# Optimization experiments

Measured on AMD Instinct MI355X. Metric: run time of the kernel, lower is better.

## Reference

```python
import jax, jax.numpy as jnp
import numpy as np

N_QUBITS = 12
N_LAYERS = 3


def _apply_ry(state, theta, q):
    # state: (2,)*n real statevector; RY on qubit q
    c = jnp.cos(theta * 0.5)
    s = jnp.sin(theta * 0.5)
    st = jnp.moveaxis(state, q, 0)
    st = jnp.stack([c * st[0] - s * st[1], s * st[0] + c * st[1]])
    return jnp.moveaxis(st, 0, q)


def _apply_cz(state, q, r):
    st = jnp.moveaxis(state, (q, r), (0, 1))
    st = st.at[1, 1].multiply(-1.0)
    return jnp.moveaxis(st, (0, 1), (q, r))


def _embed(x, params):
    # angle-embedding ansatz: L layers of RY(theta[l,q]+x[q]) + CZ ring
    n = N_QUBITS
    state = jnp.zeros((2,) * n, dtype=x.dtype).at[(0,) * n].set(1.0)
    for l in range(N_LAYERS):
        for q in range(n):
            state = _apply_ry(state, params[l, q] + x[q], q)
        for q in range(n):
            state = _apply_cz(state, q, (q + 1) % n)
    return state.reshape(-1)  # (2^n,)


def setup_inputs() -> dict:
    key = jax.random.key(0)
    k1, k2, k3 = jax.random.split(key, 3)
    data = jax.random.uniform(k1, (2048, N_QUBITS), dtype=jnp.float32)
    labels = jax.random.randint(k2, (2048,), 0, 2, dtype=jnp.int32)
    params = jax.random.normal(k3, (N_LAYERS, N_QUBITS), dtype=jnp.float32)
    return {"data": data, "labels": labels, "params": params}


def reference(data, labels, params):
    # Psi[i] = U(x_i, params)|0>, k_ij = |<psi_j|psi_i>|^2 (== prob of amp 0 of U^dag(x_j)U(x_i)|0>)
    psi = jax.vmap(_embed, in_axes=(0, None))(data, params)  # (N, 2^n)
    K = jnp.square(psi @ psi.T)                              # (N, N) pairwise kernel
    lab = 2.0 * labels.astype(psi.dtype) - 1.0               # {0,1} -> {-1,+1}
    LL = jnp.outer(lab, lab)
    kernel_polarity = jnp.sum(LL * K)
    square_sum_k = jnp.sum(K * K)
    square_sum_l = jnp.sum(LL * LL)
    return kernel_polarity / jnp.sqrt(square_sum_k * square_sum_l)
```

## Files before the change

### kernel.cpp

```cpp
#include <hip/hip_runtime.h>
#include <math.h>

#define NQ    12
#define DIM   4096
#define K_EXT 4096
#define KSL   512
#define NSAMP 2048
#define NLAY  3
#define NT2   16
#define NTRI2 136
#define NSLICE 8
#define BK    64

typedef __attribute__((ext_vector_type(8)))  short bf16x8;
typedef __attribute__((ext_vector_type(16))) float floatx16;

__device__ __forceinline__ unsigned short f32_to_bf16(float x) {
    unsigned u = __builtin_bit_cast(unsigned, x);
    u += 0x7FFFu + ((u >> 16) & 1u);
    return (unsigned short)(u >> 16);
}

__device__ __forceinline__ void gl_lds16(const unsigned short* g, unsigned short* l) {
    __builtin_amdgcn_global_load_lds(
        (const __attribute__((address_space(1))) unsigned int*)g,
        (__attribute__((address_space(3))) unsigned int*)l,
        16, 0, 0);
}

__device__ __forceinline__ void tri_decode(int bid, int& bi, int& bj) {
    int i = (int)((33.0 - sqrt(33.0*33.0 - 8.0*(double)bid)) * 0.5);
    int start = i*(33-i)/2;
    while (bid < start)               { --i; start = i*(33-i)/2; }
    while (bid >= start + (NT2 - i))  { start += NT2 - i; ++i; }
    bi = i; bj = i + (bid - start);
}

__global__ __launch_bounds__(256) void sim_kernel(const float* __restrict__ data,
                                                  const float* __restrict__ params,
                                                  unsigned short* __restrict__ pe)
{
    __shared__ float CS[2*36], SN[2*36];
    __shared__ float trans[2][4608];
    const int tid  = threadIdx.x;
    const int wave = tid >> 6, lane = tid & 63;
    const int sidx = wave >> 1;
    const int w    = wave & 1;
    const int smp  = blockIdx.x * 2 + sidx;

    if (w == 0 && lane < NLAY*NQ) {
        const int q = lane % NQ;
        const float th = 0.5f * (params[lane] + data[smp*NQ + q]);
        CS[sidx*36 + lane] = cosf(th);
        SN[sidx*36 + lane] = sinf(th);
    }
    __syncthreads();

    float v[32];
    #pragma unroll
    for (int r = 0; r < 32; ++r) v[r] = 0.f;
    if (w == 0 && lane == 0) v[0] = 1.f;

    float* buf = trans[sidx];
    float* wb  = buf + 36*lane + 2304*w;
    const float* rb = buf + ((lane>>2)&15) + 16*w + 36*(lane&3);

    #pragma unroll 1
    for (int l = 0; l < NLAY; ++l) {
        const float* cs = &CS[sidx*36 + l*NQ];
        const float* sn = &SN[sidx*36 + l*NQ];
        const int even = !(l & 1);

        {
            const int qb = even ? 7 : 2;
            #pragma unroll
            for (int b = 0; b < 5; ++b) {
                const float c = cs[qb + b], s = sn[qb + b];
                const int M = 1 << b;
                #pragma unroll
                for (int r = 0; r < 32; ++r) {
                    if (!(r & M)) {
                        const float a0 = v[r], a1 = v[r | M];
                        v[r]     = c * a0 - s * a1;
                        v[r | M] = s * a0 + c * a1;
                    }
                }
            }
        }
        {
            const float c0 = cs[0], s0 = sn[0];
            const float t0 = (lane & 1) ? s0 : -s0;
            #pragma unroll
            for (int r = 0; r < 32; ++r) {
                const int iv = __builtin_bit_cast(int, v[r]);
                const int pv = __builtin_amdgcn_update_dpp(0, iv, 0xB1, 0xF, 0xF, true);
                v[r] = c0 * v[r] + t0 * __builtin_bit_cast(float, pv);
            }
            const float c1 = cs[1], s1 = sn[1];
            const float t1 = (lane & 2) ? s1 : -s1;
            #pragma unroll
            for (int r = 0; r < 32; ++r) {
                const int iv = __builtin_bit_cast(int, v[r]);
                const int pv = __builtin_amdgcn_update_dpp(0, iv, 0x4E, 0xF, 0xF, true);
                v[r] = c1 * v[r] + t1 * __builtin_bit_cast(float, pv);
            }
        }
        __syncthreads();
        #pragma unroll
        for (int t = 0; t < 8; ++t) {
            float4 q4;
            q4.x = v[4*t]; q4.y = v[4*t+1]; q4.z = v[4*t+2]; q4.w = v[4*t+3];
            *(float4*)&wb[4*t] = q4;
        }
        __syncthreads();
        #pragma unroll
        for (int r = 0; r < 32; ++r)
            v[r] = rb[144*(r & 15) + 2304*(r >> 4)];

        {
            const int qb = even ? 2 : 7;
            #pragma unroll
            for (int b = 0; b < 5; ++b) {
                const float c = cs[qb + b], s = sn[qb + b];
                const int M = 1 << b;
                #pragma unroll
                for (int r = 0; r < 32; ++r) {
                    if (!(r & M)) {
                        const float a0 = v[r], a1 = v[r | M];
                        v[r]     = c * a0 - s * a1;
                        v[r | M] = s * a0 + c * a1;
                    }
                }
            }
        }
        {
            const int Base = even ? ((lane & 3) | (((lane >> 2) & 15) << 7) | (w << 11))
                                  : (lane | (w << 6));
            const int shift = even ? 2 : 7;
            #pragma unroll
            for (int r = 0; r < 32; ++r) {
                const int i  = Base | (r << shift);
                const int t  = ((i >> 1) | (i << 11)) & 0xFFF;
                const int p  = __popc(i & t) & 1;
                v[r] = __builtin_bit_cast(float, __builtin_bit_cast(int, v[r]) ^ (p << 31));
            }
        }
    }

    const int sw = smp & 7;
    const int ell = w*64 + lane;
    unsigned short* outb = pe + (size_t)smp * K_EXT;
    #pragma unroll
    for (int c = 0; c < 4; ++c) {
        uint4 H;
        H.x = (unsigned)f32_to_bf16(v[c*8+0]) | ((unsigned)f32_to_bf16(v[c*8+1]) << 16);
        H.y = (unsigned)f32_to_bf16(v[c*8+2]) | ((unsigned)f32_to_bf16(v[c*8+3]) << 16);
        H.z = (unsigned)f32_to_bf16(v[c*8+4]) | ((unsigned)f32_to_bf16(v[c*8+5]) << 16);
        H.w = (unsigned)f32_to_bf16(v[c*8+6]) | ((unsigned)f32_to_bf16(v[c*8+7]) << 16);
        const int gc  = 4*ell + c;
        const int pos = (gc & ~7) | ((gc ^ sw) & 7);
        *(uint4*)&outb[pos*8] = H;
    }
}

__global__ __launch_bounds__(256) void gram_partial(const unsigned short* __restrict__ pe,
                                                    float* __restrict__ Gp)
{
    __shared__ __align__(16) unsigned short stage[2][2*128*64];

    const int tid   = threadIdx.x;
    const int tile  = blockIdx.x >> 3;
    const int slice = blockIdx.x & 7;
    int bi, bj; tri_decode(tile, bi, bj);
    const int k0 = slice * KSL;

    const int wave = tid >> 6, lane = tid & 63;
    const int qr = (wave >> 1) * 64;
    const int qc = (wave &  1) * 64;
    const int mrow = lane & 31;
    const int chsel = lane >> 5;
    const int sw = mrow & 7;

    floatx16 c00, c01, c10, c11;
    #pragma unroll
    for (int i = 0; i < 16; ++i) { c00[i]=0.f; c01[i]=0.f; c10[i]=0.f; c11[i]=0.f; }

    const int mat  = wave >> 1;
    const int half = wave & 1;
    const unsigned short* gbase = pe
        + ((size_t)((mat ? bj : bi)*128 + half*64 + (lane >> 3))) * K_EXT
        + k0 + (lane & 7)*8;
    const int lofs = mat*128*64 + half*64*64;

    {
        unsigned short* l = &stage[0][lofs];
        #pragma unroll
        for (int i = 0; i < 8; ++i)
            gl_lds16(gbase + (size_t)i*8*K_EXT, l + i*512);
    }
    __syncthreads();

    int cur = 0;
    #pragma unroll 1
    for (int kk = 0; kk < KSL; kk += BK) {
        if (kk + BK < KSL) {
            unsigned short* l = &stage[cur ^ 1][lofs];
            const unsigned short* g = gbase + kk + BK;
            #pragma unroll
            for (int i = 0; i < 8; ++i)
                gl_lds16(g + (size_t)i*8*K_EXT, l + i*512);
        }

        const unsigned short* As = &stage[cur][0];
        const unsigned short* Bs = &stage[cur][128*64];
        #pragma unroll
        for (int ks = 0; ks < 4; ++ks) {
            const int ch = (ks*2 + chsel) ^ sw;
            const bf16x8 a0 = *(const bf16x8*)&As[(qr +      mrow)*64 + ch*8];
            const bf16x8 a1 = *(const bf16x8*)&As[(qr + 32 + mrow)*64 + ch*8];
            const bf16x8 b0 = *(const bf16x8*)&Bs[(qc +      mrow)*64 + ch*8];
            const bf16x8 b1 = *(const bf16x8*)&Bs[(qc + 32 + mrow)*64 + ch*8];
            c00 = __builtin_amdgcn_mfma_f32_32x32x16_bf16(a0, b0, c00, 0, 0, 0);
            c01 = __builtin_amdgcn_mfma_f32_32x32x16_bf16(a0, b1, c01, 0, 0, 0);
            c10 = __builtin_amdgcn_mfma_f32_32x32x16_bf16(a1, b0, c10, 0, 0, 0);
            c11 = __builtin_amdgcn_mfma_f32_32x32x16_bf16(a1, b1, c11, 0, 0, 0);
        }
        __syncthreads();
        cur ^= 1;
    }

    float* Gt = Gp + ((size_t)slice * NTRI2 + tile) * 16384;
    const int crow = chsel * 4;
    const int ccol = lane & 31;
    #pragma unroll
    for (int rr = 0; rr < 16; ++rr) {
        const int rl = (rr & 3) + 8*(rr >> 2) + crow;
        const int r0 = qr + rl,  r1 = qr + 32 + rl;
        const int cA = qc + ccol, cB = qc + 32 + ccol;
        Gt[r0*128 + cA] = c00[rr];
        Gt[r0*128 + cB] = c01[rr];
        Gt[r1*128 + cA] = c10[rr];
        Gt[r1*128 + cB] = c11[rr];
    }
}

__global__ __launch_bounds__(256) void gram_reduce(const float* __restrict__ Gp,
                                                   const int* __restrict__ labels,
                                                   double* __restrict__ part1,
                                                   double* __restrict__ part2)
{
    __shared__ float la[128], lb[128];
    __shared__ double red[256];
    const int tid  = threadIdx.x;
    const int tile = blockIdx.x >> 2;
    const int quar = blockIdx.x & 3;
    int bi, bj; tri_decode(tile, bi, bj);

    if (tid < 128) la[tid]       = 2.0f*(float)labels[bi*128 + tid]       - 1.0f;
    else           lb[tid - 128] = 2.0f*(float)labels[bj*128 + tid - 128] - 1.0f;
    __syncthreads();

    const size_t stride = (size_t)NTRI2 * 16384;
    const float* g0 = Gp + (size_t)tile * 16384 + quar * 4096;

    double s1 = 0.0, s2 = 0.0;
    #pragma unroll 2
    for (int u = 0; u < 16; ++u) {
        const int e  = u*256 + tid;
        const int ge = quar*4096 + e;
        float g = 0.f;
        #pragma unroll
        for (int s = 0; s < NSLICE; ++s) g += g0[e + (size_t)s*stride];
        const int row = ge >> 7, col = ge & 127;
        const float w = (bi < bj) ? 2.0f : ((row < col) ? 2.0f : ((row == col) ? 1.0f : 0.0f));
        const float g2 = g * g;
        s1 += (double)(w * la[row] * lb[col] * g2);
        const double d = (double)g2;
        s2 += (double)w * d * d;
    }

    red[tid] = s1; __syncthreads();
    for (int off = 128; off; off >>= 1) { if (tid < off) red[tid] += red[tid+off]; __syncthreads(); }
    if (tid == 0) part1[blockIdx.x] = red[0];
    __syncthreads();
    red[tid] = s2; __syncthreads();
    for (int off = 128; off; off >>= 1) { if (tid < off) red[tid] += red[tid+off]; __syncthreads(); }
    if (tid == 0) part2[blockIdx.x] = red[0];
}

__global__ __launch_bounds__(256) void finalize_kernel(const double* __restrict__ part1,
                                                       const double* __restrict__ part2,
                                                       float* __restrict__ out)
{
    __shared__ double r1[256], r2[256];
    const int tid = threadIdx.x;
    double a = 0.0, b = 0.0;
    #pragma unroll
    for (int u = 0; u < 3; ++u) {
        const int s = tid + u*256;
        if (s < NTRI2*4) { a += part1[s]; b += part2[s]; }
    }
    r1[tid] = a; r2[tid] = b; __syncthreads();
    for (int off = 128; off; off >>= 1) {
        if (tid < off) { r1[tid] += r1[tid+off]; r2[tid] += r2[tid+off]; }
        __syncthreads();
    }
    if (tid == 0) out[0] = (float)(r1[0] / (sqrt(r2[0]) * (double)NSAMP));
}

extern "C" void kernel_launch(void* const* d_in, const int* in_sizes, int n_in,
                              void* d_out, int out_size, void* d_ws, size_t ws_size,
                              hipStream_t stream)
{
    const float* data   = (const float*)d_in[0];
    const int*   labels = (const int*)d_in[1];
    const float* params = (const float*)d_in[2];

    double* part1 = (double*)d_ws;
    double* part2 = part1 + 768;
    unsigned short* psi_ext = (unsigned short*)((char*)d_ws + 16384);
    float* Gp = (float*)((char*)d_ws + 16384 + (size_t)NSAMP*K_EXT*2);

    sim_kernel<<<NSAMP/2, 256, 0, stream>>>(data, params, psi_ext);
    gram_partial<<<NTRI2*NSLICE, 256, 0, stream>>>(psi_ext, Gp);
    gram_reduce<<<NTRI2*4, 256, 0, stream>>>(Gp, labels, part1, part2);
    finalize_kernel<<<1, 256, 0, stream>>>(part1, part2, (float*)d_out);
}
```

Baseline: 124.9 us.

## Compute first layer as product state, fuse finalize into reduce via atomics

The first ansatz layer acts on |0>, so it is built directly as a product state: each amplitude is a product of per-qubit cos/sin factors. The CZ ring is then applied as a parity sign flip, which skips one layer of RY butterflies and transposes. The final scalar reduction moves into gram_reduce using double atomics and a last-block counter, removing the finalize launch. gram_reduce also reads float4 vectors and does both sums in one combined tree. The accumulators are reset inside sim_kernel, which relies on kernel ordering within the stream.

```diff
diff --git a/kernel.cpp b/kernel.cpp
--- a/kernel.cpp
+++ b/kernel.cpp
@@ -38,7 +38,9 @@
 
 __global__ __launch_bounds__(256) void sim_kernel(const float* __restrict__ data,
                                                   const float* __restrict__ params,
-                                                  unsigned short* __restrict__ pe)
+                                                  unsigned short* __restrict__ pe,
+                                                  double* __restrict__ acc,
+                                                  unsigned* __restrict__ cnt)
 {
     __shared__ float CS[2*36], SN[2*36];
     __shared__ float trans[2][4608];
@@ -48,6 +50,10 @@
     const int w    = wave & 1;
     const int smp  = blockIdx.x * 2 + sidx;
 
+    if (blockIdx.x == 0 && tid == 0) {
+        acc[0] = 0.0; acc[1] = 0.0; cnt[0] = 0u;
+    }
+
     if (w == 0 && lane < NLAY*NQ) {
         const int q = lane % NQ;
         const float th = 0.5f * (params[lane] + data[smp*NQ + q]);
@@ -57,16 +63,46 @@
     __syncthreads();
 
     float v[32];
-    #pragma unroll
-    for (int r = 0; r < 32; ++r) v[r] = 0.f;
-    if (w == 0 && lane == 0) v[0] = 1.f;
 
     float* buf = trans[sidx];
     float* wb  = buf + 36*lane + 2304*w;
     const float* rb = buf + ((lane>>2)&15) + 16*w + 36*(lane&3);
 
+    {
+        const float* cs = &CS[sidx*36];
+        const float* sn = &SN[sidx*36];
+        const int hi = (lane >> 2) & 15;
+        float fx = ((lane & 1) ? sn[0] : cs[0]) * ((lane & 2) ? sn[1] : cs[1]);
+        fx *= ((hi & 1) ? sn[7]  : cs[7]);
+        fx *= ((hi & 2) ? sn[8]  : cs[8]);
+        fx *= ((hi & 4) ? sn[9]  : cs[9]);
+        fx *= ((hi & 8) ? sn[10] : cs[10]);
+        fx *= (w ? sn[11] : cs[11]);
+        v[0] = fx * cs[2];
+        v[1] = fx * sn[2];
+        #pragma unroll
+        for (int b = 1; b < 5; ++b) {
+            const int M = 1 << b;
+            #pragma unroll
+            for (int r = 0; r < 32; ++r) {
+                if (r < M) {
+                    v[r | M] = v[r] * sn[2 + b];
+                    v[r]     = v[r] * cs[2 + b];
+                }
+            }
+        }
+        const int Base = (lane & 3) | (hi << 7) | (w << 11);
+        #pragma unroll
+        for (int r = 0; r < 32; ++r) {
+            const int i  = Base | (r << 2);
+            const int t  = ((i >> 1) | (i << 11)) & 0xFFF;
+            const int p  = __popc(i & t) & 1;
+            v[r] = __builtin_bit_cast(float, __builtin_bit_cast(int, v[r]) ^ (p << 31));
+        }
+    }
+
     #pragma unroll 1
-    for (int l = 0; l < NLAY; ++l) {
+    for (int l = 1; l < NLAY; ++l) {
         const float* cs = &CS[sidx*36 + l*NQ];
         const float* sn = &SN[sidx*36 + l*NQ];
         const int even = !(l & 1);
@@ -246,11 +282,12 @@
 
 __global__ __launch_bounds__(256) void gram_reduce(const float* __restrict__ Gp,
                                                    const int* __restrict__ labels,
-                                                   double* __restrict__ part1,
-                                                   double* __restrict__ part2)
+                                                   double* __restrict__ acc,
+                                                   unsigned* __restrict__ cnt,
+                                                   float* __restrict__ out)
 {
     __shared__ float la[128], lb[128];
-    __shared__ double red[256];
+    __shared__ double red1[256], red2[256];
     const int tid  = threadIdx.x;
     const int tile = blockIdx.x >> 2;
     const int quar = blockIdx.x & 3;
@@ -264,48 +301,46 @@
     const float* g0 = Gp + (size_t)tile * 16384 + quar * 4096;
 
     double s1 = 0.0, s2 = 0.0;
-    #pragma unroll 2
-    for (int u = 0; u < 16; ++u) {
-        const int e  = u*256 + tid;
-        const int ge = quar*4096 + e;
-        float g = 0.f;
-        #pragma unroll
-        for (int s = 0; s < NSLICE; ++s) g += g0[e + (size_t)s*stride];
-        const int row = ge >> 7, col = ge & 127;
-        const float w = (bi < bj) ? 2.0f : ((row < col) ? 2.0f : ((row == col) ? 1.0f : 0.0f));
-        const float g2 = g * g;
-        s1 += (double)(w * la[row] * lb[col] * g2);
-        const double d = (double)g2;
-        s2 += (double)w * d * d;
-    }
-
-    red[tid] = s1; __syncthreads();
-    for (int off = 128; off; off >>= 1) { if (tid < off) red[tid] += red[tid+off]; __syncthreads(); }
-    if (tid == 0) part1[blockIdx.x] = red[0];
-    __syncthreads();
-    red[tid] = s2; __syncthreads();
-    for (int off = 128; off; off >>= 1) { if (tid < off) red[tid] += red[tid+off]; __syncthreads(); }
-    if (tid == 0) part2[blockIdx.x] = red[0];
-}
-
-__global__ __launch_bounds__(256) void finalize_kernel(const double* __restrict__ part1,
-                                                       const double* __restrict__ part2,
-                                                       float* __restrict__ out)
-{
-    __shared__ double r1[256], r2[256];
-    const int tid = threadIdx.x;
-    double a = 0.0, b = 0.0;
     #pragma unroll
-    for (int u = 0; u < 3; ++u) {
-        const int s = tid + u*256;
-        if (s < NTRI2*4) { a += part1[s]; b += part2[s]; }
-    }
-    r1[tid] = a; r2[tid] = b; __syncthreads();
+    for (int u = 0; u < 4; ++u) {
+        const int e = u*1024 + tid*4;
+        float4 g = make_float4(0.f, 0.f, 0.f, 0.f);
+        #pragma unroll
+        for (int s = 0; s < NSLICE; ++s) {
+            const float4 t = *(const float4*)&g0[e + (size_t)s*stride];
+            g.x += t.x; g.y += t.y; g.z += t.z; g.w += t.w;
+        }
+        const int ge  = quar*4096 + e;
+        const int row = ge >> 7, c0 = ge & 127;
+        const float lr = la[row];
+        const float gg[4] = {g.x, g.y, g.z, g.w};
+        #pragma unroll
+        for (int j = 0; j < 4; ++j) {
+            const int col = c0 + j;
+            const float w = (bi < bj) ? 2.0f : ((row < col) ? 2.0f : ((row == col) ? 1.0f : 0.0f));
+            const float g2 = gg[j] * gg[j];
+            s1 += (double)(w * lr * lb[col] * g2);
+            const double d = (double)g2;
+            s2 += (double)w * d * d;
+        }
+    }
+
+    red1[tid] = s1; red2[tid] = s2; __syncthreads();
     for (int off = 128; off; off >>= 1) {
-        if (tid < off) { r1[tid] += r1[tid+off]; r2[tid] += r2[tid+off]; }
+        if (tid < off) { red1[tid] += red1[tid+off]; red2[tid] += red2[tid+off]; }
         __syncthreads();
     }
-    if (tid == 0) out[0] = (float)(r1[0] / (sqrt(r2[0]) * (double)NSAMP));
+    if (tid == 0) {
+        atomicAdd(&acc[0], red1[0]);
+        atomicAdd(&acc[1], red2[0]);
+        __threadfence();
+        const unsigned old = atomicAdd(cnt, 1u);
+        if (old == NTRI2*4 - 1) {
+            const double t1 = atomicAdd(&acc[0], 0.0);
+            const double t2 = atomicAdd(&acc[1], 0.0);
+            out[0] = (float)(t1 / (sqrt(t2) * (double)NSAMP));
+        }
+    }
 }
 
 extern "C" void kernel_launch(void* const* d_in, const int* in_sizes, int n_in,
@@ -316,13 +351,12 @@
     const int*   labels = (const int*)d_in[1];
     const float* params = (const float*)d_in[2];
 
-    double* part1 = (double*)d_ws;
-    double* part2 = part1 + 768;
-    unsigned short* psi_ext = (unsigned short*)((char*)d_ws + 16384);
+    double*   acc = (double*)d_ws;
+    unsigned* cnt = (unsigned*)((char*)d_ws + 64);
+    unsigned short* psi = (unsigned short*)((char*)d_ws + 16384);
     float* Gp = (float*)((char*)d_ws + 16384 + (size_t)NSAMP*K_EXT*2);
 
-    sim_kernel<<<NSAMP/2, 256, 0, stream>>>(data, params, psi_ext);
-    gram_partial<<<NTRI2*NSLICE, 256, 0, stream>>>(psi_ext, Gp);
-    gram_reduce<<<NTRI2*4, 256, 0, stream>>>(Gp, labels, part1, part2);
-    finalize_kernel<<<1, 256, 0, stream>>>(part1, part2, (float*)d_out);
-}
+    sim_kernel<<<NSAMP/2, 256, 0, stream>>>(data, params, psi, acc, cnt);
+    gram_partial<<<NTRI2*NSLICE, 256, 0, stream>>>(psi, Gp);
+    gram_reduce<<<NTRI2*4, 256, 0, stream>>>(Gp, labels, acc, cnt, (float*)d_out);
+}
```

Result: slower. 138.3 us (+10.7%).

## Compute first layer analytically as product state and halve K-split slices

Applied to the files above, without the earlier changes.

The first RY layer acting on |0> yields a product state, so each amplitude is now computed directly as a product of cos/sin factors. The CZ ring then becomes a parity sign flip, which lets the simulation loop start at layer 1. Separately, the Gram K-split goes from 8 to 4 slices of 1024, which halves the partial Gram outputs and the reduction traffic. The cost is fewer blocks in gram_partial, and so less parallelism. The gram_reduce kernel was not changed, so it may still assume 8 slices.

```diff
diff --git a/kernel.cpp b/kernel.cpp
--- a/kernel.cpp
+++ b/kernel.cpp
@@ -4,12 +4,12 @@
 #define NQ    12
 #define DIM   4096
 #define K_EXT 4096
-#define KSL   512
+#define KSL   1024
 #define NSAMP 2048
 #define NLAY  3
 #define NT2   16
 #define NTRI2 136
-#define NSLICE 8
+#define NSLICE 4
 #define BK    64
 
 typedef __attribute__((ext_vector_type(8)))  short bf16x8;
@@ -57,16 +57,46 @@
     __syncthreads();
 
     float v[32];
-    #pragma unroll
-    for (int r = 0; r < 32; ++r) v[r] = 0.f;
-    if (w == 0 && lane == 0) v[0] = 1.f;
 
     float* buf = trans[sidx];
     float* wb  = buf + 36*lane + 2304*w;
     const float* rb = buf + ((lane>>2)&15) + 16*w + 36*(lane&3);
 
+    {
+        const float* cs = &CS[sidx*36];
+        const float* sn = &SN[sidx*36];
+        const int hi = (lane >> 2) & 15;
+        float fx = ((lane & 1) ? sn[0] : cs[0]) * ((lane & 2) ? sn[1] : cs[1]);
+        fx *= ((hi & 1) ? sn[7]  : cs[7]);
+        fx *= ((hi & 2) ? sn[8]  : cs[8]);
+        fx *= ((hi & 4) ? sn[9]  : cs[9]);
+        fx *= ((hi & 8) ? sn[10] : cs[10]);
+        fx *= (w ? sn[11] : cs[11]);
+        v[0] = fx * cs[2];
+        v[1] = fx * sn[2];
+        #pragma unroll
+        for (int b = 1; b < 5; ++b) {
+            const int M = 1 << b;
+            #pragma unroll
+            for (int r = 0; r < 32; ++r) {
+                if (r < M) {
+                    v[r | M] = v[r] * sn[2 + b];
+                    v[r]     = v[r] * cs[2 + b];
+                }
+            }
+        }
+        const int Base = (lane & 3) | (hi << 7) | (w << 11);
+        #pragma unroll
+        for (int r = 0; r < 32; ++r) {
+            const int i  = Base | (r << 2);
+            const int t  = ((i >> 1) | (i << 11)) & 0xFFF;
+            const int p  = __popc(i & t) & 1;
+            v[r] = __builtin_bit_cast(float, __builtin_bit_cast(int, v[r]) ^ (p << 31));
+        }
+    }
+
     #pragma unroll 1
-    for (int l = 0; l < NLAY; ++l) {
+    for (int l = 1; l < NLAY; ++l) {
         const float* cs = &CS[sidx*36 + l*NQ];
         const float* sn = &SN[sidx*36 + l*NQ];
         const int even = !(l & 1);
@@ -169,8 +199,8 @@
     __shared__ __align__(16) unsigned short stage[2][2*128*64];
 
     const int tid   = threadIdx.x;
-    const int tile  = blockIdx.x >> 3;
-    const int slice = blockIdx.x & 7;
+    const int tile  = blockIdx.x >> 2;
+    const int slice = blockIdx.x & 3;
     int bi, bj; tri_decode(tile, bi, bj);
     const int k0 = slice * KSL;
 
@@ -318,11 +348,11 @@
 
     double* part1 = (double*)d_ws;
     double* part2 = part1 + 768;
-    unsigned short* psi_ext = (unsigned short*)((char*)d_ws + 16384);
+    unsigned short* psi = (unsigned short*)((char*)d_ws + 16384);
     float* Gp = (float*)((char*)d_ws + 16384 + (size_t)NSAMP*K_EXT*2);
 
-    sim_kernel<<<NSAMP/2, 256, 0, stream>>>(data, params, psi_ext);
-    gram_partial<<<NTRI2*NSLICE, 256, 0, stream>>>(psi_ext, Gp);
+    sim_kernel<<<NSAMP/2, 256, 0, stream>>>(data, params, psi);
+    gram_partial<<<NTRI2*NSLICE, 256, 0, stream>>>(psi, Gp);
     gram_reduce<<<NTRI2*4, 256, 0, stream>>>(Gp, labels, part1, part2);
     finalize_kernel<<<1, 256, 0, stream>>>(part1, part2, (float*)d_out);
 }
```

New measurement: 124.0 us, median of 2. Within noise of the previous version (-0.7%).
